# Performance work log

Measured on AMD Instinct MI355X. Metric: run time of the kernel, lower is better.

## Reference

```python
import jax, jax.numpy as jnp
import numpy as np

N_NODES = 100000
N_EDGES = 1200000
EMBED_DIM = 64
CONV_DIMS = [64, 32, 16]
EPS = 1e-12


def setup_inputs() -> dict:
    key = jax.random.key(0)
    ks = jax.random.split(key, 16)
    def xavier(k, shape):
        fan_out, fan_in = shape
        bound = np.sqrt(6.0 / (fan_in + fan_out))
        return jax.random.uniform(k, shape, jnp.float32, -bound, bound)
    inp = {
        "entity_user_embed": jax.random.normal(ks[0], (N_NODES, EMBED_DIM), jnp.float32) * 0.1,
        "w1_0": xavier(ks[1], (64, 64)), "b1_0": jnp.zeros((64,), jnp.float32),
        "w2_0": xavier(ks[2], (64, 64)), "b2_0": jnp.zeros((64,), jnp.float32),
        "w1_1": xavier(ks[3], (32, 64)), "b1_1": jnp.zeros((32,), jnp.float32),
        "w2_1": xavier(ks[4], (32, 64)), "b2_1": jnp.zeros((32,), jnp.float32),
        "w1_2": xavier(ks[5], (16, 32)), "b1_2": jnp.zeros((16,), jnp.float32),
        "w2_2": xavier(ks[6], (16, 32)), "b2_2": jnp.zeros((16,), jnp.float32),
        "edge_val": jax.random.uniform(ks[7], (N_EDGES,), jnp.float32),
        "edge_row": jax.random.randint(ks[8], (N_EDGES,), 0, N_NODES, jnp.int32),
        "edge_col": jax.random.randint(ks[9], (N_EDGES,), 0, N_NODES, jnp.int32),
    }
    return inp


def _spmm(edge_val, edge_row, edge_col, x, n):
    # sparse A_in @ x : gather source rows, scale by edge value, scatter-add to dest
    msg = edge_val[:, None] * x[edge_col]          # [E, D]
    return jax.ops.segment_sum(msg, edge_row, num_segments=n)


def _aggregate(ego, side, w1, b1, w2, b2):
    # Aggregator: LeakyReLU(linear1(ego+side)) + LeakyReLU(linear2(ego*side))
    sum_e = jax.nn.leaky_relu((ego + side) @ w1.T + b1, negative_slope=0.01)
    bi_e = jax.nn.leaky_relu((ego * side) @ w2.T + b2, negative_slope=0.01)
    return sum_e + bi_e  # dropout is identity in eval mode


def _l2norm(x):
    n = jnp.sqrt(jnp.sum(x * x, axis=1, keepdims=True))
    return x / jnp.maximum(n, EPS)


def reference(entity_user_embed, w1_0, b1_0, w2_0, b2_0,
              w1_1, b1_1, w2_1, b2_1, w1_2, b1_2, w2_2, b2_2,
              edge_val, edge_row, edge_col):
    n = entity_user_embed.shape[0]
    layers = [(w1_0, b1_0, w2_0, b2_0), (w1_1, b1_1, w2_1, b2_1), (w1_2, b1_2, w2_2, b2_2)]
    ego = entity_user_embed
    all_embed = [ego]
    for (w1, b1, w2, b2) in layers:
        side = _spmm(edge_val, edge_row, edge_col, ego, n)
        ego = _aggregate(ego, side, w1, b1, w2, b2)
        all_embed.append(_l2norm(ego))
    return jnp.concatenate(all_embed, axis=1)  # [N, 64+64+32+16]
```

## Files before the change

kernel.cpp:

```cpp
#include <hip/hip_runtime.h>


#define NODES 100000
#define OUT_STRIDE 176

typedef _Float16 f16x8 __attribute__((ext_vector_type(8)));
typedef float f32x4 __attribute__((ext_vector_type(4)));
typedef _Float16 half4_t __attribute__((ext_vector_type(4)));
typedef unsigned long long u64;

static constexpr int NV = NODES + 1;
static constexpr int NB = 256;
static constexpr int BINH = (NODES + 255) / 256;
static constexpr int M_SCAN = BINH * NB;
static constexpr int NC1 = (M_SCAN + 1023) / 1024;
static constexpr int CAP = 4096;


__global__ __launch_bounds__(1024) void bucket_count_kernel(const int* __restrict__ rows,
                                                            int* __restrict__ gh,
                                                            int e, int chunk) {
    __shared__ int lh[BINH];
    for (int t = threadIdx.x; t < BINH; t += 1024) lh[t] = 0;
    __syncthreads();
    int b = blockIdx.x;
    int start = b * chunk, end = min(e, start + chunk);
    for (int i = start + threadIdx.x; i < end; i += 1024)
        atomicAdd(&lh[rows[i] >> 8], 1);
    __syncthreads();
    for (int t = threadIdx.x; t < BINH; t += 1024) gh[t * NB + b] = lh[t];
}

__global__ __launch_bounds__(1024) void scan_k1(const int* __restrict__ in, int* __restrict__ out,
                                                int* __restrict__ sums, int m) {
    int i = blockIdx.x * 1024 + threadIdx.x;
    int v = (i < m) ? in[i] : 0;
    int lane = threadIdx.x & 63, wid = threadIdx.x >> 6;
    int incl = v;
    #pragma unroll
    for (int off = 1; off < 64; off <<= 1) {
        int t = __shfl_up(incl, off);
        if (lane >= off) incl += t;
    }
    __shared__ int wsum[16];
    if (lane == 63) wsum[wid] = incl;
    __syncthreads();
    int woff = 0;
    for (int k = 0; k < wid; ++k) woff += wsum[k];
    if (i < m) out[i] = incl - v + woff;
    if (threadIdx.x == 1023) sums[blockIdx.x] = incl + woff;
}

__global__ __launch_bounds__(1024) void scan_k2(int* __restrict__ sums, int nc) {
    int t = threadIdx.x;
    int v = (t < nc) ? sums[t] : 0;
    int lane = t & 63, wid = t >> 6;
    int incl = v;
    #pragma unroll
    for (int off = 1; off < 64; off <<= 1) {
        int x = __shfl_up(incl, off);
        if (lane >= off) incl += x;
    }
    __shared__ int wsum[16];
    if (lane == 63) wsum[wid] = incl;
    __syncthreads();
    int woff = 0;
    for (int k = 0; k < wid; ++k) woff += wsum[k];
    if (t < nc) sums[t] = incl - v + woff;
}

__global__ __launch_bounds__(1024) void scan_k3(int* __restrict__ out, const int* __restrict__ sums,
                                                int m) {
    int i = blockIdx.x * 1024 + threadIdx.x;
    if (i < m) out[i] += sums[blockIdx.x];
}

__global__ __launch_bounds__(1024) void bucket_scatter_kernel(
    const int* __restrict__ rows, const int* __restrict__ cols, const float* __restrict__ vals,
    const int* __restrict__ ghs, u64* __restrict__ tmp, int e, int chunk) {
    __shared__ int cur[BINH];
    int b = blockIdx.x;
    for (int t = threadIdx.x; t < BINH; t += 1024) cur[t] = ghs[t * NB + b];
    __syncthreads();
    int start = b * chunk, end = min(e, start + chunk);
    for (int i = start + threadIdx.x; i < end; i += 1024) {
        int r = rows[i];
        unsigned v15 = __float2uint_rn(vals[i] * 32767.f);
        unsigned pk = (unsigned)cols[i] | (v15 << 17);
        int pos = atomicAdd(&cur[r >> 8], 1);
        tmp[pos] = ((u64)(unsigned)r << 32) | pk;
    }
}

__global__ __launch_bounds__(1024) void bucket_sort_kernel(
    const u64* __restrict__ tmp, const int* __restrict__ ghs,
    unsigned* __restrict__ sorted, int* __restrict__ row_ptr, int e) {
    __shared__ u64 ebuf[CAP];
    __shared__ int hist[256], bstart[256], cursor[256], ws4[4];
    int b = blockIdx.x, t = threadIdx.x;
    int base = ghs[b * NB];
    int endp = (b == BINH - 1) ? e : ghs[(b + 1) * NB];
    int size = min(endp - base, CAP);
    for (int i = t; i < 256; i += 1024) hist[i] = 0;
    __syncthreads();
    for (int i = t; i < size; i += 1024) {
        u64 ev = tmp[base + i];
        ebuf[i] = ev;
        atomicAdd(&hist[(int)(ev >> 32) & 255], 1);
    }
    __syncthreads();
    {
        int v = (t < 256) ? hist[t] : 0;
        int lane = t & 63, wid = t >> 6;
        int incl = v;
        #pragma unroll
        for (int off = 1; off < 64; off <<= 1) {
            int x = __shfl_up(incl, off);
            if (lane >= off) incl += x;
        }
        if (lane == 63 && wid < 4) ws4[wid] = incl;
        __syncthreads();
        if (t < 256) {
            int woff = 0;
            for (int k = 0; k < wid; ++k) woff += ws4[k];
            int ex = incl - v + woff;
            bstart[t] = ex;
            cursor[t] = ex;
            int rr = b * 256 + t;
            if (rr <= NODES) row_ptr[rr] = base + ex;
        }
    }
    __syncthreads();
    for (int i = t; i < size; i += 1024) {
        u64 ev = ebuf[i];
        int bin = (int)(ev >> 32) & 255;
        int pos = base + atomicAdd(&cursor[bin], 1);
        sorted[pos] = (unsigned)ev;
    }
}


__global__ void prep_embed_kernel(const float4* __restrict__ x4, float4* __restrict__ out4,
                                  half4_t* __restrict__ xh) {
    int i = blockIdx.x * blockDim.x + threadIdx.x;
    if (i < NODES * 16) {
        int r = i >> 4, c = i & 15;
        float4 v = x4[i];
        out4[r * (OUT_STRIDE / 4) + c] = v;
        xh[i] = half4_t{(_Float16)v.x, (_Float16)v.y, (_Float16)v.z, (_Float16)v.w};
    }
}


template <int DIN, int DOUT>
__global__ __launch_bounds__(512, 6) void layer_kernel(
    const _Float16* __restrict__ xh, const unsigned* __restrict__ edges,
    const int* __restrict__ row_ptr,
    const float* __restrict__ w1, const float* __restrict__ b1,
    const float* __restrict__ w2, const float* __restrict__ b2,
    _Float16* __restrict__ ego_out,
    float* __restrict__ outp,
    int n) {
    constexpr int KT = DIN / 32;
    constexpr int NT = DOUT / 16;
    constexpr int NFRAG = 2 * KT * NT;
    constexpr int DPL = DIN / 4;
    constexpr int C8 = DPL / 8;
    constexpr int SROWH = DIN + 8;

    __shared__ f16x8 wfrag[NFRAG * 64];
    __shared__ _Float16 tiles[8][2][16 * SROWH];

    for (int slot = threadIdx.x; slot < NFRAG * 64; slot += 512) {
        int l = slot & 63, fid = slot >> 6;
        int mat = fid / (KT * NT);
        int kt = (fid / NT) % KT;
        int nt = fid % NT;
        const float* w = mat ? w2 : w1;
        int o = nt * 16 + (l & 15);
        int kb = kt * 32 + (l >> 4) * 8;
        const float* src = w + o * DIN + kb;
        f16x8 f;
        #pragma unroll
        for (int jj = 0; jj < 8; ++jj) f[jj] = (_Float16)src[jj];
        wfrag[slot] = f;
    }
    __syncthreads();

    int wid = threadIdx.x >> 6, lane = threadIdx.x & 63;
    int g = lane >> 2, li = lane & 3;
    int q = lane >> 4, cl = lane & 15;

    float bias1[NT], bias2[NT];
    #pragma unroll
    for (int nt = 0; nt < NT; ++nt) {
        bias1[nt] = b1[nt * 16 + cl];
        bias2[nt] = b2[nt * 16 + cl];
    }

    int r0 = blockIdx.x * 128 + wid * 16;

    int r = r0 + g;
    bool valid = r < n;
    int rr = valid ? r : 0;
    int s = valid ? row_ptr[rr] : 0;
    int e = valid ? row_ptr[rr + 1] : 0;

    const _Float16* xrow = xh + (size_t)rr * DIN + li * DPL;
    f16x8 egoh[C8];
    #pragma unroll
    for (int c = 0; c < C8; ++c) egoh[c] = *(const f16x8*)(xrow + c * 8);

    f16x8 accv[C8];
    #pragma unroll
    for (int c = 0; c < C8; ++c) accv[c] = (f16x8)(_Float16)0;

    constexpr float SCL = 1.f / 32767.f;
    const _Float16* xbase = xh + li * DPL;
    int j = s;
    for (; j + 3 < e; j += 4) {
        unsigned pk[4];
        #pragma unroll
        for (int k = 0; k < 4; ++k) pk[k] = edges[j + k];
        f16x8 xv[4][C8];
        #pragma unroll
        for (int k = 0; k < 4; ++k) {
            const _Float16* p = xbase + (size_t)(pk[k] & 0x1FFFFu) * DIN;
            #pragma unroll
            for (int c = 0; c < C8; ++c) xv[k][c] = *(const f16x8*)(p + c * 8);
        }
        #pragma unroll
        for (int k = 0; k < 4; ++k) {
            _Float16 vh = (_Float16)((float)(pk[k] >> 17) * SCL);
            #pragma unroll
            for (int c = 0; c < C8; ++c)
                accv[c] += xv[k][c] * vh;
        }
    }
    for (; j < e; ++j) {
        unsigned p = edges[j];
        _Float16 vh = (_Float16)((float)(p >> 17) * SCL);
        const _Float16* xp = xbase + (size_t)(p & 0x1FFFFu) * DIN;
        #pragma unroll
        for (int c = 0; c < C8; ++c)
            accv[c] += (*(const f16x8*)(xp + c * 8)) * vh;
    }

    _Float16* srow = &tiles[wid][0][g * SROWH + li * DPL];
    _Float16* brow = &tiles[wid][1][g * SROWH + li * DPL];
    #pragma unroll
    for (int c = 0; c < C8; ++c) {
        *(f16x8*)(srow + c * 8) = egoh[c] + accv[c];
        *(f16x8*)(brow + c * 8) = egoh[c] * accv[c];
    }

    f16x8 sumA[KT], biA[KT];
    #pragma unroll
    for (int kt = 0; kt < KT; ++kt) {
        sumA[kt] = *(const f16x8*)&tiles[wid][0][cl * SROWH + kt * 32 + q * 8];
        biA[kt]  = *(const f16x8*)&tiles[wid][1][cl * SROWH + kt * 32 + q * 8];
    }

    float ov[NT][4];
    #pragma unroll
    for (int nt = 0; nt < NT; ++nt) {
        f32x4 c1 = {bias1[nt], bias1[nt], bias1[nt], bias1[nt]};
        f32x4 c2 = {bias2[nt], bias2[nt], bias2[nt], bias2[nt]};
        #pragma unroll
        for (int kt = 0; kt < KT; ++kt) {
            f16x8 wa = wfrag[((0 * KT + kt) * NT + nt) * 64 + lane];
            f16x8 wb = wfrag[((1 * KT + kt) * NT + nt) * 64 + lane];
            c1 = __builtin_amdgcn_mfma_f32_16x16x32_f16(sumA[kt], wa, c1, 0, 0, 0);
            c2 = __builtin_amdgcn_mfma_f32_16x16x32_f16(biA[kt], wb, c2, 0, 0, 0);
        }
        #pragma unroll
        for (int t = 0; t < 4; ++t) {
            float u1 = c1[t] > 0.f ? c1[t] : 0.01f * c1[t];
            float u2 = c2[t] > 0.f ? c2[t] : 0.01f * c2[t];
            ov[nt][t] = u1 + u2;
        }
    }

    #pragma unroll
    for (int t = 0; t < 4; ++t) {
        float sq = 0.f;
        #pragma unroll
        for (int nt = 0; nt < NT; ++nt) sq += ov[nt][t] * ov[nt][t];
        #pragma unroll
        for (int off = 1; off < 16; off <<= 1) sq += __shfl_xor(sq, off);
        float inv = 1.f / fmaxf(sqrtf(sq), 1e-12f);
        int rw = r0 + 4 * q + t;
        if (rw < n) {
            #pragma unroll
            for (int nt = 0; nt < NT; ++nt) {
                float o = ov[nt][t];
                if (ego_out) ego_out[(size_t)rw * DOUT + nt * 16 + cl] = (_Float16)o;
                outp[(size_t)rw * OUT_STRIDE + nt * 16 + cl] = o * inv;
            }
        }
    }
}


static size_t align_up(size_t x) { return (x + 255) & ~(size_t)255; }

extern "C" void kernel_launch(void* const* d_in, const int* in_sizes, int n_in,
                              void* d_out, int out_size, void* d_ws, size_t ws_size,
                              hipStream_t stream) {
    const float* embed = (const float*)d_in[0];
    const float* w1_0 = (const float*)d_in[1];  const float* b1_0 = (const float*)d_in[2];
    const float* w2_0 = (const float*)d_in[3];  const float* b2_0 = (const float*)d_in[4];
    const float* w1_1 = (const float*)d_in[5];  const float* b1_1 = (const float*)d_in[6];
    const float* w2_1 = (const float*)d_in[7];  const float* b2_1 = (const float*)d_in[8];
    const float* w1_2 = (const float*)d_in[9];  const float* b1_2 = (const float*)d_in[10];
    const float* w2_2 = (const float*)d_in[11]; const float* b2_2 = (const float*)d_in[12];
    const float* edge_val = (const float*)d_in[13];
    const int*   edge_row = (const int*)d_in[14];
    const int*   edge_col = (const int*)d_in[15];
    const int E = in_sizes[14];
    const int N = in_sizes[0] / 64;
    float* out = (float*)d_out;

    char* ws = (char*)d_ws;
    size_t off = 0;
    int* row_ptr   = (int*)(ws + off); off = align_up(off + (size_t)NV * 4);
    int* gh        = (int*)(ws + off); off = align_up(off + (size_t)M_SCAN * 4);
    int* ghs       = (int*)(ws + off); off = align_up(off + (size_t)M_SCAN * 4);
    int* sums      = (int*)(ws + off); off = align_up(off + (size_t)256 * 4);
    u64* tmp       = (u64*)(ws + off); off = align_up(off + (size_t)E * 8);
    unsigned* sorted = (unsigned*)(ws + off); off = align_up(off + (size_t)E * 4);
    _Float16* embed_h = (_Float16*)(ws + off); off = align_up(off + (size_t)N * 64 * 2);
    _Float16* ego1_h  = (_Float16*)(ws + off); off = align_up(off + (size_t)N * 64 * 2);
    _Float16* ego2_h  = (_Float16*)(ws + off); off = align_up(off + (size_t)N * 32 * 2);
    (void)ws_size; (void)n_in; (void)out_size;

    int chunk = (E + NB - 1) / NB;
    bucket_count_kernel<<<NB, 1024, 0, stream>>>(edge_row, gh, E, chunk);
    scan_k1<<<NC1, 1024, 0, stream>>>(gh, ghs, sums, M_SCAN);
    scan_k2<<<1, 1024, 0, stream>>>(sums, NC1);
    scan_k3<<<NC1, 1024, 0, stream>>>(ghs, sums, M_SCAN);
    bucket_scatter_kernel<<<NB, 1024, 0, stream>>>(edge_row, edge_col, edge_val, ghs, tmp, E, chunk);
    bucket_sort_kernel<<<BINH, 1024, 0, stream>>>(tmp, ghs, sorted, row_ptr, E);

    prep_embed_kernel<<<(N * 16 + 255) / 256, 256, 0, stream>>>(
        (const float4*)embed, (float4*)out, (half4_t*)embed_h);

    int lb = (N + 127) / 128;
    layer_kernel<64, 64><<<lb, 512, 0, stream>>>(embed_h, sorted, row_ptr,
        w1_0, b1_0, w2_0, b2_0, ego1_h, out + 64, N);
    layer_kernel<64, 32><<<lb, 512, 0, stream>>>(ego1_h, sorted, row_ptr,
        w1_1, b1_1, w2_1, b2_1, ego2_h, out + 128, N);
    layer_kernel<32, 16><<<lb, 512, 0, stream>>>(ego2_h, sorted, row_ptr,
        w1_2, b1_2, w2_2, b2_2, nullptr, out + 160, N);
}
```

Baseline: 133.5 us.

## Gather neighbor rows directly in MFMA operand layout, dropping LDS transpose tiles

```diff
diff --git a/kernel.cpp b/kernel.cpp
--- a/kernel.cpp
+++ b/kernel.cpp
@@ -153,7 +153,7 @@
 
 
 template <int DIN, int DOUT>
-__global__ __launch_bounds__(512, 6) void layer_kernel(
+__global__ __launch_bounds__(512, 8) void layer_kernel(
     const _Float16* __restrict__ xh, const unsigned* __restrict__ edges,
     const int* __restrict__ row_ptr,
     const float* __restrict__ w1, const float* __restrict__ b1,
@@ -164,12 +164,8 @@
     constexpr int KT = DIN / 32;
     constexpr int NT = DOUT / 16;
     constexpr int NFRAG = 2 * KT * NT;
-    constexpr int DPL = DIN / 4;
-    constexpr int C8 = DPL / 8;
-    constexpr int SROWH = DIN + 8;
 
     __shared__ f16x8 wfrag[NFRAG * 64];
-    __shared__ _Float16 tiles[8][2][16 * SROWH];
 
     for (int slot = threadIdx.x; slot < NFRAG * 64; slot += 512) {
         int l = slot & 63, fid = slot >> 6;
@@ -188,77 +184,60 @@
     __syncthreads();
 
     int wid = threadIdx.x >> 6, lane = threadIdx.x & 63;
-    int g = lane >> 2, li = lane & 3;
     int q = lane >> 4, cl = lane & 15;
 
-    float bias1[NT], bias2[NT];
-    #pragma unroll
-    for (int nt = 0; nt < NT; ++nt) {
-        bias1[nt] = b1[nt * 16 + cl];
-        bias2[nt] = b2[nt * 16 + cl];
-    }
-
     int r0 = blockIdx.x * 128 + wid * 16;
-
-    int r = r0 + g;
+    int r = r0 + cl;
     bool valid = r < n;
     int rr = valid ? r : 0;
     int s = valid ? row_ptr[rr] : 0;
     int e = valid ? row_ptr[rr + 1] : 0;
 
-    const _Float16* xrow = xh + (size_t)rr * DIN + li * DPL;
-    f16x8 egoh[C8];
-    #pragma unroll
-    for (int c = 0; c < C8; ++c) egoh[c] = *(const f16x8*)(xrow + c * 8);
-
-    f16x8 accv[C8];
-    #pragma unroll
-    for (int c = 0; c < C8; ++c) accv[c] = (f16x8)(_Float16)0;
+    f16x8 accv[KT];
+    #pragma unroll
+    for (int ck = 0; ck < KT; ++ck) accv[ck] = (f16x8)(_Float16)0;
 
     constexpr float SCL = 1.f / 32767.f;
-    const _Float16* xbase = xh + li * DPL;
+    const _Float16* xq = xh + q * 8;
     int j = s;
     for (; j + 3 < e; j += 4) {
         unsigned pk[4];
         #pragma unroll
         for (int k = 0; k < 4; ++k) pk[k] = edges[j + k];
-        f16x8 xv[4][C8];
         #pragma unroll
         for (int k = 0; k < 4; ++k) {
-            const _Float16* p = xbase + (size_t)(pk[k] & 0x1FFFFu) * DIN;
-            #pragma unroll
-            for (int c = 0; c < C8; ++c) xv[k][c] = *(const f16x8*)(p + c * 8);
-        }
-        #pragma unroll
-        for (int k = 0; k < 4; ++k) {
+            const _Float16* p = xq + (size_t)(pk[k] & 0x1FFFFu) * DIN;
             _Float16 vh = (_Float16)((float)(pk[k] >> 17) * SCL);
             #pragma unroll
-            for (int c = 0; c < C8; ++c)
-                accv[c] += xv[k][c] * vh;
+            for (int ck = 0; ck < KT; ++ck)
+                accv[ck] += (*(const f16x8*)(p + ck * 32)) * vh;
         }
     }
     for (; j < e; ++j) {
         unsigned p = edges[j];
         _Float16 vh = (_Float16)((float)(p >> 17) * SCL);
-        const _Float16* xp = xbase + (size_t)(p & 0x1FFFFu) * DIN;
-        #pragma unroll
-        for (int c = 0; c < C8; ++c)
-            accv[c] += (*(const f16x8*)(xp + c * 8)) * vh;
-    }
-
-    _Float16* srow = &tiles[wid][0][g * SROWH + li * DPL];
-    _Float16* brow = &tiles[wid][1][g * SROWH + li * DPL];
-    #pragma unroll
-    for (int c = 0; c < C8; ++c) {
-        *(f16x8*)(srow + c * 8) = egoh[c] + accv[c];
-        *(f16x8*)(brow + c * 8) = egoh[c] * accv[c];
+        const _Float16* xp = xq + (size_t)(p & 0x1FFFFu) * DIN;
+        #pragma unroll
+        for (int ck = 0; ck < KT; ++ck)
+            accv[ck] += (*(const f16x8*)(xp + ck * 32)) * vh;
     }
 
     f16x8 sumA[KT], biA[KT];
-    #pragma unroll
-    for (int kt = 0; kt < KT; ++kt) {
-        sumA[kt] = *(const f16x8*)&tiles[wid][0][cl * SROWH + kt * 32 + q * 8];
-        biA[kt]  = *(const f16x8*)&tiles[wid][1][cl * SROWH + kt * 32 + q * 8];
+    {
+        const _Float16* er = xq + (size_t)rr * DIN;
+        #pragma unroll
+        for (int ck = 0; ck < KT; ++ck) {
+            f16x8 eg = *(const f16x8*)(er + ck * 32);
+            sumA[ck] = eg + accv[ck];
+            biA[ck]  = eg * accv[ck];
+        }
+    }
+
+    float bias1[NT], bias2[NT];
+    #pragma unroll
+    for (int nt = 0; nt < NT; ++nt) {
+        bias1[nt] = b1[nt * 16 + cl];
+        bias2[nt] = b2[nt * 16 + cl];
     }
 
     float ov[NT][4];
```

New measurement: 145.1 us. +8.7%, slower.

## Reorder nodes by degree within each 256-row bin for layer balance

Applied to the files above, without the earlier changes.

```diff
diff --git a/kernel.cpp b/kernel.cpp
--- a/kernel.cpp
+++ b/kernel.cpp
@@ -94,14 +94,18 @@
 
 __global__ __launch_bounds__(1024) void bucket_sort_kernel(
     const u64* __restrict__ tmp, const int* __restrict__ ghs,
-    unsigned* __restrict__ sorted, int* __restrict__ row_ptr, int e) {
+    unsigned* __restrict__ sorted, int* __restrict__ row_ptr,
+    int* __restrict__ perm, int e) {
     __shared__ u64 ebuf[CAP];
-    __shared__ int hist[256], bstart[256], cursor[256], ws4[4];
+    __shared__ int hist[256], cursor[256], ws4[4];
+    __shared__ int dh[64];
     int b = blockIdx.x, t = threadIdx.x;
     int base = ghs[b * NB];
     int endp = (b == BINH - 1) ? e : ghs[(b + 1) * NB];
     int size = min(endp - base, CAP);
+    int nvalid = min(256, NODES - b * 256);
     for (int i = t; i < 256; i += 1024) hist[i] = 0;
+    if (t < 64) dh[t] = 0;
     __syncthreads();
     for (int i = t; i < size; i += 1024) {
         u64 ev = tmp[base + i];
@@ -124,11 +128,25 @@
             int woff = 0;
             for (int k = 0; k < wid; ++k) woff += ws4[k];
             int ex = incl - v + woff;
-            bstart[t] = ex;
             cursor[t] = ex;
             int rr = b * 256 + t;
             if (rr <= NODES) row_ptr[rr] = base + ex;
         }
+    }
+    int deg = 0;
+    if (t < nvalid) {
+        deg = min(hist[t], 63);
+        atomicAdd(&dh[deg], 1);
+    }
+    __syncthreads();
+    if (t == 0) {
+        int run = 0;
+        for (int d = 63; d >= 0; --d) { int x = dh[d]; dh[d] = run; run += x; }
+    }
+    __syncthreads();
+    if (t < nvalid) {
+        int pos = atomicAdd(&dh[deg], 1);
+        perm[b * 256 + pos] = b * 256 + t;
     }
     __syncthreads();
     for (int i = t; i < size; i += 1024) {
@@ -155,7 +173,7 @@
 template <int DIN, int DOUT>
 __global__ __launch_bounds__(512, 6) void layer_kernel(
     const _Float16* __restrict__ xh, const unsigned* __restrict__ edges,
-    const int* __restrict__ row_ptr,
+    const int* __restrict__ row_ptr, const int* __restrict__ perm,
     const float* __restrict__ w1, const float* __restrict__ b1,
     const float* __restrict__ w2, const float* __restrict__ b2,
     _Float16* __restrict__ ego_out,
@@ -200,13 +218,13 @@
 
     int r0 = blockIdx.x * 128 + wid * 16;
 
-    int r = r0 + g;
-    bool valid = r < n;
-    int rr = valid ? r : 0;
-    int s = valid ? row_ptr[rr] : 0;
-    int e = valid ? row_ptr[rr + 1] : 0;
-
-    const _Float16* xrow = xh + (size_t)rr * DIN + li * DPL;
+    int slot = r0 + g;
+    bool valid = slot < n;
+    int r = valid ? perm[slot] : 0;
+    int s = valid ? row_ptr[r] : 0;
+    int e = valid ? row_ptr[r + 1] : 0;
+
+    const _Float16* xrow = xh + (size_t)r * DIN + li * DPL;
     f16x8 egoh[C8];
     #pragma unroll
     for (int c = 0; c < C8; ++c) egoh[c] = *(const f16x8*)(xrow + c * 8);
@@ -289,8 +307,9 @@
         #pragma unroll
         for (int off = 1; off < 16; off <<= 1) sq += __shfl_xor(sq, off);
         float inv = 1.f / fmaxf(sqrtf(sq), 1e-12f);
-        int rw = r0 + 4 * q + t;
-        if (rw < n) {
+        int slot_w = r0 + 4 * q + t;
+        if (slot_w < n) {
+            int rw = perm[slot_w];
             #pragma unroll
             for (int nt = 0; nt < NT; ++nt) {
                 float o = ov[nt][t];
@@ -324,6 +343,7 @@
     char* ws = (char*)d_ws;
     size_t off = 0;
     int* row_ptr   = (int*)(ws + off); off = align_up(off + (size_t)NV * 4);
+    int* perm      = (int*)(ws + off); off = align_up(off + (size_t)NODES * 4);
     int* gh        = (int*)(ws + off); off = align_up(off + (size_t)M_SCAN * 4);
     int* ghs       = (int*)(ws + off); off = align_up(off + (size_t)M_SCAN * 4);
     int* sums      = (int*)(ws + off); off = align_up(off + (size_t)256 * 4);
@@ -340,16 +360,16 @@
     scan_k2<<<1, 1024, 0, stream>>>(sums, NC1);
     scan_k3<<<NC1, 1024, 0, stream>>>(ghs, sums, M_SCAN);
     bucket_scatter_kernel<<<NB, 1024, 0, stream>>>(edge_row, edge_col, edge_val, ghs, tmp, E, chunk);
-    bucket_sort_kernel<<<BINH, 1024, 0, stream>>>(tmp, ghs, sorted, row_ptr, E);
+    bucket_sort_kernel<<<BINH, 1024, 0, stream>>>(tmp, ghs, sorted, row_ptr, perm, E);
 
     prep_embed_kernel<<<(N * 16 + 255) / 256, 256, 0, stream>>>(
         (const float4*)embed, (float4*)out, (half4_t*)embed_h);
 
     int lb = (N + 127) / 128;
-    layer_kernel<64, 64><<<lb, 512, 0, stream>>>(embed_h, sorted, row_ptr,
+    layer_kernel<64, 64><<<lb, 512, 0, stream>>>(embed_h, sorted, row_ptr, perm,
         w1_0, b1_0, w2_0, b2_0, ego1_h, out + 64, N);
-    layer_kernel<64, 32><<<lb, 512, 0, stream>>>(ego1_h, sorted, row_ptr,
+    layer_kernel<64, 32><<<lb, 512, 0, stream>>>(ego1_h, sorted, row_ptr, perm,
         w1_1, b1_1, w2_1, b2_1, ego2_h, out + 128, N);
-    layer_kernel<32, 16><<<lb, 512, 0, stream>>>(ego2_h, sorted, row_ptr,
+    layer_kernel<32, 16><<<lb, 512, 0, stream>>>(ego2_h, sorted, row_ptr, perm,
         w1_2, b1_2, w2_2, b2_2, nullptr, out + 160, N);
 }
```

Result: slower. 144.8 us (+8.4%).
